# Performance work log

Measured on AMD Instinct MI355X. Metric: run time of the kernel, lower is better.

## Reference

```python
import jax, jax.numpy as jnp
import numpy as np

T, P, S, A = 16384, 64, 128, 16
VD, VO, TD, TO, H = 1024, 256, 768, 256, 512

def _mlp1(x, w1, b1, w2, b2):
    # MLP1: Linear(d,d) -> ReLU -> Linear(d,out)
    return jax.nn.relu(x @ w1 + b1) @ w2 + b2

def setup_inputs() -> dict:
    key = jax.random.key(0)
    ks = jax.random.split(key, 20)
    p = lambda i, shape: jax.random.normal(ks[i], shape, jnp.float32) * 0.02
    return {
        "video": jax.random.normal(ks[0], (T, VD), jnp.float32),
        "para": jax.random.normal(ks[1], (P, TD), jnp.float32),
        "question": jax.random.normal(ks[2], (1, TD), jnp.float32),
        "paras_score": jax.random.normal(ks[3], (P,), jnp.float32),
        "a_texts": jax.random.normal(ks[4], (S, A, TD), jnp.float32),
        "a_buttons": jax.random.normal(ks[5], (S, A, VD), jnp.float32),
        "timestamps": jnp.sort(jax.random.randint(ks[6], (P, 2), 0, T), axis=1),
        # mlp_v: VD -> VD -> VO
        "wv1": p(7, (VD, VD)), "bv1": jnp.zeros(VD, jnp.float32),
        "wv2": p(8, (VD, VO)), "bv2": jnp.zeros(VO, jnp.float32),
        # mlp_t: TD -> TD -> TO
        "wt1": p(9, (TD, TD)), "bt1": jnp.zeros(TD, jnp.float32),
        "wt2": p(10, (TD, TO)), "bt2": jnp.zeros(TO, jnp.float32),
        # mlp_pre: (2*VO+2*TO) -> same -> H
        "wp1": p(11, (2*VO+2*TO, 2*VO+2*TO)), "bp1": jnp.zeros(2*VO+2*TO, jnp.float32),
        "wp2": p(12, (2*VO+2*TO, H)), "bp2": jnp.zeros(H, jnp.float32),
        # GRUCell H -> H (torch layout: [3H, H])
        "w_ih": p(13, (3*H, H)), "b_ih": jnp.zeros(3*H, jnp.float32),
        "w_hh": p(14, (3*H, H)), "b_hh": jnp.zeros(3*H, jnp.float32),
        # proj: H -> H -> 1
        "wj1": p(15, (H, H)), "bj1": jnp.zeros(H, jnp.float32),
        "wj2": p(16, (H, 1)), "bj2": jnp.zeros(1, jnp.float32),
        "state0": jax.random.normal(ks[17], (H,), jnp.float32),
    }

def reference(video, para, question, paras_score, a_texts, a_buttons, timestamps,
              wv1, bv1, wv2, bv2, wt1, bt1, wt2, bt2, wp1, bp1, wp2, bp2,
              w_ih, b_ih, w_hh, b_hh, wj1, bj1, wj2, bj2, state0):
    score = jax.nn.softmax(paras_score)                       # [P]
    video_v = _mlp1(video, wv1, bv1, wv2, bv2)                # [T, VO]
    # segment mean pooling over ragged [start, end) spans; start>=end -> single frame
    s = timestamps[:, 0]
    e = jnp.maximum(timestamps[:, 1], s + 1)
    idx = jnp.arange(video.shape[0])
    mask = ((idx[None, :] >= s[:, None]) & (idx[None, :] < e[:, None])).astype(video_v.dtype)  # [P, T]
    seg = (mask @ video_v) / (e - s).astype(video_v.dtype)[:, None]  # [P, VO]
    video_seg = score @ seg                                   # [VO]
    text_seg = score @ _mlp1(para, wt1, bt1, wt2, bt2)        # [TO]
    q = _mlp1(question, wt1, bt1, wt2, bt2)                   # [1, TO]
    qa = q[None] + _mlp1(a_texts, wt1, bt1, wt2, bt2)         # [S, A, TO]
    btn = _mlp1(a_buttons, wv1, bv1, wv2, bv2)                # [S, A, VO]
    Sn, An = qa.shape[0], qa.shape[1]
    vb = jnp.broadcast_to(video_seg, (Sn, An, video_seg.shape[0]))
    tb = jnp.broadcast_to(text_seg, (Sn, An, text_seg.shape[0]))
    inputs_pre = _mlp1(jnp.concatenate([vb, tb, qa, btn], axis=-1), wp1, bp1, wp2, bp2)  # [S, A, H]

    def step(state, x):  # x: [A, H]
        h = jnp.broadcast_to(state, x.shape)
        gi = x @ w_ih.T + b_ih
        gh = h @ w_hh.T + b_hh
        ir, iz, inn = jnp.split(gi, 3, axis=-1)
        hr, hz, hn = jnp.split(gh, 3, axis=-1)
        r = jax.nn.sigmoid(ir + hr)
        z = jax.nn.sigmoid(iz + hz)
        n = jnp.tanh(inn + r * hn)
        h_new = (1.0 - z) * n + z * h                          # [A, H]
        logits = _mlp1(h_new, wj1, bj1, wj2, bj2)[:, 0]        # [A]
        new_state = x[jnp.argmax(logits)]                      # history 'max' update
        return new_state, logits

    _, scores = jax.lax.scan(step, state0, inputs_pre)
    return scores  # [S, A]
```

## Files before the change

kernel.cpp:

```cpp
#include <hip/hip_runtime.h>
#include <math.h>

#define T_FRAMES 16384
#define S_N   128
#define VD    1024
#define VO    256
#define TD    768
#define TO    256
#define HH    512
#define NTXT  2113
#define NCAND 32528
#define NGRP  2033
#define NASC  2049
#define MVB   18432

typedef __attribute__((ext_vector_type(8))) short s8v;
typedef __attribute__((ext_vector_type(4))) short s4v;
typedef __attribute__((ext_vector_type(4))) float f32x4;

__device__ __forceinline__ float bf2f(short h) {
    return __builtin_bit_cast(float, ((unsigned)(unsigned short)h) << 16);
}
__device__ __forceinline__ void split_rn(float v, short& h, short& l) {
    unsigned u = __builtin_bit_cast(unsigned, v);
    unsigned short uh = (unsigned short)((u + 0x7fff + ((u >> 16) & 1)) >> 16);
    float lf = v - bf2f((short)uh);
    unsigned ul = __builtin_bit_cast(unsigned, lf);
    unsigned short us = (unsigned short)((ul + 0x7fff + ((ul >> 16) & 1)) >> 16);
    h = (short)uh; l = (short)us;
}
__device__ __forceinline__ void gload16(const void* g, void* l) {
    __builtin_amdgcn_global_load_lds(
        (const __attribute__((address_space(1))) unsigned int*)g,
        (__attribute__((address_space(3))) unsigned int*)l, 16, 0, 0);
}
__device__ __forceinline__ f32x4 ld4s(const short* __restrict__ H,
                                      const short* __restrict__ L, size_t o) {
    s4v h = *(const s4v*)(H + o);
    s4v l = *(const s4v*)(L + o);
    return (f32x4){bf2f(h[0]) + bf2f(l[0]), bf2f(h[1]) + bf2f(l[1]),
                   bf2f(h[2]) + bf2f(l[2]), bf2f(h[3]) + bf2f(l[3])};
}
__device__ __forceinline__ float sigm(float x) { return 1.f / (1.f + expf(-x)); }

struct GD {
    const short *Ah, *Al, *Bh, *Bl;
    const float *bias;
    short *Ch, *Cl;
    int M, N, K, gx, nblk, relu;
};

template<int MODE, int BKL>
__global__ __launch_bounds__((BKL == 64 ? 512 : 256), 2) void mgemm3(
    GD d0, GD d1,
    const float* __restrict__ wt, float* __restrict__ uacc,
    const float* __restrict__ wj2, float* __restrict__ LG)
{
    constexpr int NTH = (BKL == 64) ? 512 : 256;
    constexpr int GPR = BKL / 8;
    constexpr int TSH = 128 * BKL;
    constexpr int MF  = (BKL == 64) ? 2 : 4;
    constexpr int WMs = MF * 16;
    __shared__ __align__(16) short lds[2 * 4 * TSH];

    const int tid = threadIdx.x;
    const int nwg = gridDim.x;
    const int orig = blockIdx.x;
    const int qq = nwg >> 3, r8 = nwg & 7, xcd = orig & 7, ridx = orig >> 3;
    const int swz = (xcd < r8 ? xcd * (qq + 1) : r8 * (qq + 1) + (xcd - r8) * qq) + ridx;

    GD d; int pid;
    if (swz < d0.nblk) { d = d0; pid = swz; } else { d = d1; pid = swz - d0.nblk; }
    const int bm = (pid / d.gx) * 128;
    const int bn = (pid % d.gx) * 128;

    const int wv = tid >> 6, l = tid & 63;
    const int fr = l & 15, fg = l >> 4;
    const int wr = wv >> 1, wc = wv & 1;

    f32x4 acc[MF][4];
#pragma unroll
    for (int m = 0; m < MF; ++m)
#pragma unroll
        for (int n = 0; n < 4; ++n) acc[m][n] = (f32x4){0.f, 0.f, 0.f, 0.f};

    auto stage = [&](int buf, int k0) {
        short* base = &lds[buf * 4 * TSH];
#pragma unroll
        for (int i = 0; i < (128 * GPR) / NTH; ++i) {
            int g = i * NTH + tid;
            int row = g / GPR, c = g % GPR;
            int cs = (BKL == 32) ? (c ^ ((row >> 1) & 3)) : (c ^ (row & 7));
            int ga = bm + row; if (ga > d.M - 1) ga = d.M - 1;
            size_t ao = (size_t)ga * d.K + k0 + cs * 8;
            size_t bo = (size_t)(bn + row) * d.K + k0 + cs * 8;
            gload16(d.Ah + ao, base + 0 * TSH + g * 8);
            gload16(d.Al + ao, base + 1 * TSH + g * 8);
            gload16(d.Bh + bo, base + 2 * TSH + g * 8);
            gload16(d.Bl + bo, base + 3 * TSH + g * 8);
        }
    };
    auto compute = [&](int buf) {
        const short* base = &lds[buf * 4 * TSH];
#pragma unroll
        for (int s = 0; s < BKL / 32; ++s) {
            s8v ah[MF], al[MF];
#pragma unroll
            for (int m = 0; m < MF; ++m) {
                int row = wr * WMs + m * 16 + fr;
                int sw = (BKL == 32) ? ((row >> 1) & 3) : (row & 7);
                int off = row * BKL + (((s << 2) + fg) ^ sw) * 8;
                ah[m] = *(const s8v*)&base[0 * TSH + off];
                al[m] = *(const s8v*)&base[1 * TSH + off];
            }
#pragma unroll
            for (int n = 0; n < 4; ++n) {
                int col = wc * 64 + n * 16 + fr;
                int sw = (BKL == 32) ? ((col >> 1) & 3) : (col & 7);
                int off = col * BKL + (((s << 2) + fg) ^ sw) * 8;
                s8v bh = *(const s8v*)&base[2 * TSH + off];
                s8v bl = *(const s8v*)&base[3 * TSH + off];
#pragma unroll
                for (int m = 0; m < MF; ++m) {
                    f32x4 c = acc[m][n];
                    c = __builtin_amdgcn_mfma_f32_16x16x32_bf16(al[m], bh, c, 0, 0, 0);
                    c = __builtin_amdgcn_mfma_f32_16x16x32_bf16(ah[m], bl, c, 0, 0, 0);
                    c = __builtin_amdgcn_mfma_f32_16x16x32_bf16(ah[m], bh, c, 0, 0, 0);
                    acc[m][n] = c;
                }
            }
        }
    };

    stage(0, 0);
    __syncthreads();
    const int nk = d.K / BKL;
    int cur = 0;
    for (int t = 0; t < nk; ++t) {
        if (t + 1 < nk) stage(cur ^ 1, (t + 1) * BKL);
        compute(cur);
        __syncthreads();
        cur ^= 1;
    }

    if (MODE == 2 && bm < 16384) {
        float wtv[MF][4];
#pragma unroll
        for (int m = 0; m < MF; ++m)
#pragma unroll
            for (int r = 0; r < 4; ++r)
                wtv[m][r] = wt[bm + wr * WMs + m * 16 + fg * 4 + r];
#pragma unroll
        for (int n = 0; n < 4; ++n) {
            int gcol = bn + wc * 64 + n * 16 + fr;
            float bv = d.bias[gcol];
            float s = 0.f;
#pragma unroll
            for (int m = 0; m < MF; ++m)
#pragma unroll
                for (int r = 0; r < 4; ++r)
                    s += fmaxf(acc[m][n][r] + bv, 0.f) * wtv[m][r];
            s += __shfl_xor(s, 16);
            s += __shfl_xor(s, 32);
            if (fg == 0) atomicAdd(&uacc[gcol], s);
        }
        return;
    }
    if (MODE == 3) {
#pragma unroll
        for (int m = 0; m < MF; ++m) {
            float sv[4] = {0.f, 0.f, 0.f, 0.f};
#pragma unroll
            for (int n = 0; n < 4; ++n) {
                int gcol = bn + wc * 64 + n * 16 + fr;
                float bv = d.bias[gcol], w2 = wj2[gcol];
#pragma unroll
                for (int r = 0; r < 4; ++r)
                    sv[r] += fmaxf(acc[m][n][r] + bv, 0.f) * w2;
            }
#pragma unroll
            for (int r = 0; r < 4; ++r) {
                float v = sv[r];
                v += __shfl_xor(v, 1); v += __shfl_xor(v, 2);
                v += __shfl_xor(v, 4); v += __shfl_xor(v, 8);
                int gm = bm + wr * WMs + m * 16 + fg * 4 + r;
                if (fr == 0 && gm < d.M) atomicAdd(&LG[gm], v);
            }
        }
        return;
    }
    {
        const int rowoff = (MODE == 2) ? 16384 : 0;
#pragma unroll
        for (int n = 0; n < 4; ++n) {
            int gcol = bn + wc * 64 + n * 16 + fr;
            float bv = d.bias[gcol];
#pragma unroll
            for (int m = 0; m < MF; ++m) {
                int rbase = bm + wr * WMs + m * 16 + fg * 4;
#pragma unroll
                for (int r = 0; r < 4; ++r) {
                    int gm = rbase + r;
                    if (gm < d.M) {
                        float v = acc[m][n][r] + bv;
                        if (d.relu || MODE == 2) v = fmaxf(v, 0.f);
                        short hh, ll; split_rn(v, hh, ll);
                        size_t o = (size_t)(gm - rowoff) * d.N + gcol;
                        d.Ch[o] = hh; d.Cl[o] = ll;
                    }
                }
            }
        }
    }
}

struct PrepArgs {
    const float* src[9];
    short* dh[9]; short* dl[9];
    int K[9], N[9], tr[9];
};
__global__ __launch_bounds__(256) void prep_weights(PrepArgs a)
{
    const int wi = blockIdx.y;
    const float* src = a.src[wi];
    short* dh = a.dh[wi]; short* dl = a.dl[wi];
    const int K = a.K[wi], N = a.N[wi];
    __shared__ float t[32][33];
    if (a.tr[wi]) {
        int nb = N >> 5, kb = K >> 5;
        if ((int)blockIdx.x >= nb * kb) return;
        int tx = threadIdx.x & 31, ty = threadIdx.x >> 5;
        int n0 = ((int)blockIdx.x % nb) << 5, k0 = ((int)blockIdx.x / nb) << 5;
#pragma unroll
        for (int i = 0; i < 4; ++i)
            t[ty + 8 * i][tx] = src[(size_t)(k0 + ty + 8 * i) * N + n0 + tx];
        __syncthreads();
#pragma unroll
        for (int i = 0; i < 4; ++i) {
            int n = n0 + ty + 8 * i, k = k0 + tx;
            short h, l; split_rn(t[tx][ty + 8 * i], h, l);
            dh[(size_t)n * K + k] = h;
            dl[(size_t)n * K + k] = l;
        }
    } else {
        int total = K * N;
        int i0 = ((int)blockIdx.x * 256 + (int)threadIdx.x) * 4;
        if (i0 < total) {
            float4 v = *(const float4*)(src + i0);
            float vv[4] = {v.x, v.y, v.z, v.w};
#pragma unroll
            for (int e = 0; e < 4; ++e) {
                short h, l; split_rn(vv[e], h, l);
                dh[i0 + e] = h; dl[i0 + e] = l;
            }
        }
    }
}

__global__ __launch_bounds__(256) void asplit_vb(const float* __restrict__ video,
                                                 const float* __restrict__ btns,
                                                 short* __restrict__ h,
                                                 short* __restrict__ l)
{
    const size_t vtotal = (size_t)16384 * VD;
    const size_t total = (size_t)MVB * VD;
    for (size_t i = ((size_t)blockIdx.x * 256 + threadIdx.x) * 4; i < total;
         i += (size_t)gridDim.x * 1024) {
        const float* s = (i < vtotal) ? video + i : btns + (i - vtotal);
        float4 v = *(const float4*)s;
        float vv[4] = {v.x, v.y, v.z, v.w};
#pragma unroll
        for (int e = 0; e < 4; ++e) {
            short hh, ll; split_rn(vv[e], hh, ll);
            h[i + e] = hh; l[i + e] = ll;
        }
    }
}

__global__ __launch_bounds__(256) void prolog(const float* __restrict__ ps,
                                              float* __restrict__ sc,
                                              float* __restrict__ u,
                                              const float* __restrict__ state0,
                                              short* __restrict__ ASCh,
                                              short* __restrict__ ASCl,
                                              const float* __restrict__ bj2,
                                              float* __restrict__ LG)
{
    int b = blockIdx.x, tid = threadIdx.x;
    if (b == 0) {
        if (tid < 64) {
            float x = ps[tid];
            float m = x;
            for (int off = 32; off; off >>= 1) m = fmaxf(m, __shfl_xor(m, off));
            float e = expf(x - m);
            float s = e;
            for (int off = 32; off; off >>= 1) s += __shfl_xor(s, off);
            sc[tid] = e / s;
        }
    } else if (b == 1) {
#pragma unroll
        for (int i = 0; i < 4; ++i) u[tid + i * 256] = 0.f;
    } else if (b == 2) {
#pragma unroll
        for (int i = 0; i < 2; ++i) {
            int c = tid + i * 256;
            short h, l; split_rn(state0[c], h, l);
            ASCh[c] = h; ASCl[c] = l;
        }
    } else {
        int i = (b - 3) * 256 + tid;
        if (i < NCAND) LG[i] = bj2[0];
    }
}

__global__ __launch_bounds__(256) void wt_kernel(const int* __restrict__ ts,
                                                 const float* __restrict__ sc,
                                                 float* __restrict__ wt)
{
    __shared__ int ss[64], se[64];
    __shared__ float sw[64];
    int tid = threadIdx.x;
    if (tid < 64) {
        int s = ts[2 * tid];
        int e = ts[2 * tid + 1];
        if (e < s + 1) e = s + 1;
        ss[tid] = s; se[tid] = e;
        sw[tid] = sc[tid] / (float)(e - s);
    }
    __syncthreads();
    int t = blockIdx.x * 256 + tid;
    if (t < T_FRAMES) {
        float w = 0.f;
#pragma unroll
        for (int p = 0; p < 64; ++p)
            if (t >= ss[p] && t < se[p]) w += sw[p];
        wt[t] = w;
    }
}

__global__ __launch_bounds__(256) void mkbias2(const float* __restrict__ u,
                                               const float* __restrict__ wv2,
                                               const float* __restrict__ bv2,
                                               const float* __restrict__ sc,
                                               const short* __restrict__ T2h,
                                               const short* __restrict__ T2l,
                                               const float* __restrict__ bp1,
                                               const float* __restrict__ wp1,
                                               float* __restrict__ bias2)
{
    __shared__ float vs[256], ts[256];
    int tid = threadIdx.x;
    float a = 0.f;
    for (int p = 0; p < 64; ++p) {
        size_t o = (size_t)p * TO + tid;
        a = fmaf(sc[p], bf2f(T2h[o]) + bf2f(T2l[o]), a);
    }
    ts[tid] = a;
    float b = bv2[tid];
    for (int i = 0; i < VD; ++i)
        b = fmaf(u[i], wv2[(size_t)i * VO + tid], b);
    vs[tid] = b;
    __syncthreads();
    int j = blockIdx.x * 256 + tid;
    float acc = bp1[j];
    for (int i = 0; i < 256; ++i) acc = fmaf(vs[i], wp1[(size_t)i * 1024 + j], acc);
    for (int i = 0; i < 256; ++i) acc = fmaf(ts[i], wp1[(size_t)(256 + i) * 1024 + j], acc);
    bias2[j] = acc;
}

__global__ __launch_bounds__(256) void copy_xt_split(const float* __restrict__ para,
                                                     const float* __restrict__ question,
                                                     const float* __restrict__ atexts,
                                                     short* __restrict__ Xh,
                                                     short* __restrict__ Xl)
{
    size_t total = (size_t)NTXT * TD;
    for (size_t id = ((size_t)blockIdx.x * 256 + threadIdx.x) * 4; id < total;
         id += (size_t)gridDim.x * 1024) {
        int r = (int)(id / TD);
        int c = (int)(id - (size_t)r * TD);
        const float* s;
        if (r < 64)       s = para + (size_t)r * TD + c;
        else if (r == 64) s = question + c;
        else              s = atexts + (size_t)(r - 65) * TD + c;
        float4 v = *(const float4*)s;
        float vv[4] = {v.x, v.y, v.z, v.w};
#pragma unroll
        for (int e = 0; e < 4; ++e) {
            short h, l; split_rn(vv[e], h, l);
            Xh[id + e] = h; Xl[id + e] = l;
        }
    }
}

__global__ __launch_bounds__(256) void xp_build_split(const short* __restrict__ T2h,
                                                      const short* __restrict__ T2l,
                                                      const short* __restrict__ btnh,
                                                      const short* __restrict__ btnl,
                                                      short* __restrict__ Xh,
                                                      short* __restrict__ Xl)
{
    int idx = blockIdx.x * 256 + threadIdx.x;
    int r = idx >> 7;
    int c = (idx & 127) << 2;
    s4v h, l;
    if (c < 256) {
        size_t o1 = (size_t)64 * TO + c;
        size_t o2 = (size_t)(65 + r) * TO + c;
        s4v h1 = *(const s4v*)(T2h + o1), l1 = *(const s4v*)(T2l + o1);
        s4v h2 = *(const s4v*)(T2h + o2), l2 = *(const s4v*)(T2l + o2);
#pragma unroll
        for (int e = 0; e < 4; ++e) {
            float v = (bf2f(h1[e]) + bf2f(l1[e])) + (bf2f(h2[e]) + bf2f(l2[e]));
            short hh, ll; split_rn(v, hh, ll);
            h[e] = hh; l[e] = ll;
        }
    } else {
        size_t o = (size_t)r * VO + (c - 256);
        h = *(const s4v*)(btnh + o);
        l = *(const s4v*)(btnl + o);
    }
    size_t out = (size_t)r * 512 + c;
    *(s4v*)(Xh + out) = h;
    *(s4v*)(Xl + out) = l;
}

__global__ __launch_bounds__(256) void hn_build(const short* __restrict__ GIh,
                                                const short* __restrict__ GIl,
                                                const short* __restrict__ GHh,
                                                const short* __restrict__ GHl,
                                                const short* __restrict__ ASCh,
                                                const short* __restrict__ ASCl,
                                                short* __restrict__ HNh,
                                                short* __restrict__ HNl)
{
    const int total = NCAND * 128;
    for (int gid = blockIdx.x * 256 + threadIdx.x; gid < total;
         gid += gridDim.x * 256) {
        int r = gid >> 7;
        int c = (gid & 127) << 2;
        int crow, girow;
        if (r < 16) { crow = 0; girow = r; }
        else {
            int rr = r - 16;
            int k  = 1 + (rr >> 8);
            int rem = rr & 255;
            int ci = rem >> 4;
            int aa = rem & 15;
            crow = 1 + (k - 1) * 16 + ci;
            girow = k * 16 + aa;
        }
        size_t gi0 = (size_t)girow * 1536 + c;
        size_t gh0 = (size_t)crow * 1536 + c;
        f32x4 ir = ld4s(GIh, GIl, gi0);
        f32x4 iz = ld4s(GIh, GIl, gi0 + 512);
        f32x4 in = ld4s(GIh, GIl, gi0 + 1024);
        f32x4 hr = ld4s(GHh, GHl, gh0);
        f32x4 hz = ld4s(GHh, GHl, gh0 + 512);
        f32x4 hn = ld4s(GHh, GHl, gh0 + 1024);
        f32x4 h  = ld4s(ASCh, ASCl, (size_t)crow * HH + c);
        s4v oh, ol;
#pragma unroll
        for (int e = 0; e < 4; ++e) {
            float rg = sigm(ir[e] + hr[e]);
            float z  = sigm(iz[e] + hz[e]);
            float n  = tanhf(in[e] + rg * hn[e]);
            float v  = (1.f - z) * n + z * h[e];
            short hh, ll; split_rn(v, hh, ll);
            oh[e] = hh; ol[e] = ll;
        }
        size_t out = (size_t)r * HH + c;
        *(s4v*)(HNh + out) = oh;
        *(s4v*)(HNl + out) = ol;
    }
}

__global__ __launch_bounds__(256) void argmax16(const float* __restrict__ LG,
                                                int* __restrict__ idx)
{
    int g = blockIdx.x * 4 + (threadIdx.x >> 6);
    if (g >= NGRP) return;
    int lane = threadIdx.x & 63;
    float v = (lane < 16) ? LG[g * 16 + lane] : -INFINITY;
    int bi = (lane < 16) ? lane : 16;
    for (int off = 8; off >= 1; off >>= 1) {
        float ov = __shfl_xor(v, off);
        int   oi = __shfl_xor(bi, off);
        if (ov > v || (ov == v && oi < bi)) { v = ov; bi = oi; }
    }
    if (lane == 0) idx[g] = bi;
}

__global__ void chase2(const float* __restrict__ LG, const int* __restrict__ idx,
                       float* __restrict__ out)
{
    int lane = threadIdx.x;
    int g = 0;
    for (int k = 0; k < S_N; ++k) {
        if (lane < 16) out[k * 16 + lane] = LG[g * 16 + lane];
        int ci = idx[g];
        g = 1 + k * 16 + ci;
    }
}

extern "C" void kernel_launch(void* const* d_in, const int* in_sizes, int n_in,
                              void* d_out, int out_size, void* d_ws, size_t ws_size,
                              hipStream_t stream)
{
    const float* video      = (const float*)d_in[0];
    const float* para       = (const float*)d_in[1];
    const float* question   = (const float*)d_in[2];
    const float* paras_scr  = (const float*)d_in[3];
    const float* a_texts    = (const float*)d_in[4];
    const float* a_buttons  = (const float*)d_in[5];
    const int*   timestamps = (const int*)d_in[6];
    const float* wv1 = (const float*)d_in[7];
    const float* bv1 = (const float*)d_in[8];
    const float* wv2 = (const float*)d_in[9];
    const float* bv2 = (const float*)d_in[10];
    const float* wt1 = (const float*)d_in[11];
    const float* bt1 = (const float*)d_in[12];
    const float* wt2 = (const float*)d_in[13];
    const float* bt2 = (const float*)d_in[14];
    const float* wp1 = (const float*)d_in[15];
    const float* bp1 = (const float*)d_in[16];
    const float* wp2 = (const float*)d_in[17];
    const float* bp2 = (const float*)d_in[18];
    const float* w_ih = (const float*)d_in[19];
    const float* b_ih = (const float*)d_in[20];
    const float* w_hh = (const float*)d_in[21];
    const float* b_hh = (const float*)d_in[22];
    const float* wj1 = (const float*)d_in[23];
    const float* bj1 = (const float*)d_in[24];
    const float* wj2 = (const float*)d_in[25];
    const float* bj2 = (const float*)d_in[26];
    const float* state0 = (const float*)d_in[27];

    char* wsb = (char*)d_ws;
    size_t off = 0;
    auto alloc = [&](size_t bytes) -> char* {
        size_t o = (off + 255) & ~(size_t)255;
        off = o + bytes;
        return wsb + o;
    };
    auto allocF = [&](size_t n) -> float* { return (float*)alloc(n * 4); };
    auto allocS = [&](size_t n) -> short* { return (short*)alloc(n * 2); };
    auto allocI = [&](size_t n) -> int*   { return (int*)alloc(n * 4); };

    float* sc    = allocF(64);
    float* wtb   = allocF(T_FRAMES);
    float* u     = allocF(VD);
    float* bias2 = allocF(1024);
    float* LG    = allocF(NCAND);
    int*   amx   = allocI(NGRP);

    short* Avbh = allocS((size_t)MVB * VD);
    short* Avbl = allocS((size_t)MVB * VD);
    short* H1bh = allocS((size_t)2048 * VD);
    short* H1bl = allocS((size_t)2048 * VD);
    short* Xth  = allocS((size_t)NTXT * TD);
    short* Xtl  = allocS((size_t)NTXT * TD);
    short* T1h  = allocS((size_t)NTXT * TD);
    short* T1l  = allocS((size_t)NTXT * TD);
    short* T2h  = allocS((size_t)NTXT * TO);
    short* T2l  = allocS((size_t)NTXT * TO);
    short* btnh = allocS((size_t)2048 * VO);
    short* btnl = allocS((size_t)2048 * VO);
    short* Xph  = allocS((size_t)2048 * 512);
    short* Xpl  = allocS((size_t)2048 * 512);
    short* P1h  = allocS((size_t)2048 * 1024);
    short* P1l  = allocS((size_t)2048 * 1024);
    short* ASCh = allocS((size_t)NASC * HH);
    short* ASCl = allocS((size_t)NASC * HH);
    short* GIh  = allocS((size_t)2048 * 1536);
    short* GIl  = allocS((size_t)2048 * 1536);
    short* GHh  = allocS((size_t)NASC * 1536);
    short* GHl  = allocS((size_t)NASC * 1536);
    short* IPh  = ASCh + HH;
    short* IPl  = ASCl + HH;
    short* HNh  = Avbh;
    short* HNl  = Avbl;

    short* wv1Th = allocS((size_t)VD * VD);    short* wv1Tl = allocS((size_t)VD * VD);
    short* wt1Th = allocS((size_t)TD * TD);    short* wt1Tl = allocS((size_t)TD * TD);
    short* wt2Th = allocS((size_t)TO * TD);    short* wt2Tl = allocS((size_t)TO * TD);
    short* wv2Th = allocS((size_t)VO * VD);    short* wv2Tl = allocS((size_t)VO * VD);
    short* wp1Th = allocS((size_t)1024 * 512); short* wp1Tl = allocS((size_t)1024 * 512);
    short* wp2Th = allocS((size_t)HH * 1024);  short* wp2Tl = allocS((size_t)HH * 1024);
    short* wj1Th = allocS((size_t)HH * HH);    short* wj1Tl = allocS((size_t)HH * HH);
    short* wihSh = allocS((size_t)1536 * HH);  short* wihSl = allocS((size_t)1536 * HH);
    short* whhSh = allocS((size_t)1536 * HH);  short* whhSl = allocS((size_t)1536 * HH);

    GD gE; gE.Ah = gE.Al = gE.Bh = gE.Bl = nullptr; gE.bias = nullptr;
    gE.Ch = gE.Cl = nullptr; gE.M = gE.N = gE.K = gE.gx = gE.nblk = gE.relu = 0;

    prolog<<<131, 256, 0, stream>>>(paras_scr, sc, u, state0, ASCh, ASCl, bj2, LG);
    wt_kernel<<<T_FRAMES / 256, 256, 0, stream>>>(timestamps, sc, wtb);
    {
        PrepArgs pa;
        const float* s[9] = {wv1, wt1, wt2, wv2, wp1 + (size_t)512 * 1024, wp2, wj1, w_ih, w_hh};
        short* dh[9] = {wv1Th, wt1Th, wt2Th, wv2Th, wp1Th, wp2Th, wj1Th, wihSh, whhSh};
        short* dl[9] = {wv1Tl, wt1Tl, wt2Tl, wv2Tl, wp1Tl, wp2Tl, wj1Tl, wihSl, whhSl};
        int K[9] = {VD, TD, TD, VD, 512, 1024, HH, HH, HH};
        int N[9] = {VD, TD, TO, VO, 1024, HH, HH, 1536, 1536};
        int tr[9] = {1, 1, 1, 1, 1, 1, 1, 0, 0};
        for (int i = 0; i < 9; ++i) {
            pa.src[i] = s[i]; pa.dh[i] = dh[i]; pa.dl[i] = dl[i];
            pa.K[i] = K[i]; pa.N[i] = N[i]; pa.tr[i] = tr[i];
        }
        prep_weights<<<dim3(1024, 9), 256, 0, stream>>>(pa);
    }
    asplit_vb<<<4608, 256, 0, stream>>>(video, a_buttons, Avbh, Avbl);
    copy_xt_split<<<1586, 256, 0, stream>>>(para, question, a_texts, Xth, Xtl);

    {
        GD g1{Avbh, Avbl, wv1Th, wv1Tl, bv1, H1bh, H1bl, MVB, VD, VD, 8, 1152, 1};
        mgemm3<2, 32><<<1152, 256, 0, stream>>>(g1, gE, wtb, u, nullptr, nullptr);
    }
    {
        GD g2{H1bh, H1bl, wv2Th, wv2Tl, bv2, btnh, btnl, 2048, VO, VD, 2, 32, 0};
        GD g3{Xth, Xtl, wt1Th, wt1Tl, bt1, T1h, T1l, NTXT, TD, TD, 6, 102, 1};
        mgemm3<0, 64><<<134, 512, 0, stream>>>(g2, g3, nullptr, nullptr, nullptr, nullptr);
    }
    {
        GD g4{T1h, T1l, wt2Th, wt2Tl, bt2, T2h, T2l, NTXT, TO, TD, 2, 34, 0};
        mgemm3<0, 64><<<34, 512, 0, stream>>>(g4, gE, nullptr, nullptr, nullptr, nullptr);
    }
    mkbias2<<<4, 256, 0, stream>>>(u, wv2, bv2, sc, T2h, T2l, bp1, wp1, bias2);
    xp_build_split<<<1024, 256, 0, stream>>>(T2h, T2l, btnh, btnl, Xph, Xpl);
    {
        GD g5{Xph, Xpl, wp1Th, wp1Tl, bias2, P1h, P1l, 2048, 1024, 512, 8, 128, 1};
        mgemm3<0, 64><<<128, 512, 0, stream>>>(g5, gE, nullptr, nullptr, nullptr, nullptr);
    }
    {
        GD g6{P1h, P1l, wp2Th, wp2Tl, bp2, IPh, IPl, 2048, HH, 1024, 4, 64, 0};
        mgemm3<0, 64><<<64, 512, 0, stream>>>(g6, gE, nullptr, nullptr, nullptr, nullptr);
    }
    {
        GD g7{IPh, IPl, wihSh, wihSl, b_ih, GIh, GIl, 2048, 1536, HH, 12, 192, 0};
        GD g8{ASCh, ASCl, whhSh, whhSl, b_hh, GHh, GHl, NASC, 1536, HH, 12, 204, 0};
        mgemm3<0, 64><<<396, 512, 0, stream>>>(g7, g8, nullptr, nullptr, nullptr, nullptr);
    }
    hn_build<<<4096, 256, 0, stream>>>(GIh, GIl, GHh, GHl, ASCh, ASCl, HNh, HNl);
    {
        GD g9{HNh, HNl, wj1Th, wj1Tl, bj1, nullptr, nullptr, NCAND, HH, HH, 4, 1020, 0};
        mgemm3<3, 32><<<1020, 256, 0, stream>>>(g9, gE, nullptr, nullptr, wj2, LG);
    }
    argmax16<<<(NGRP + 3) / 4, 256, 0, stream>>>(LG, amx);
    chase2<<<1, 64, 0, stream>>>(LG, amx, (float*)d_out);
}
```

Baseline: 656.9 us.

## Merge independent GEMM launches, parallelize bias precompute, single-buffer BK32 GEMM

Turns the GEMM epilogue mode into a runtime field so GEMMs with different epilogues share one launch: the big video MLP layer now runs alongside the text first layer, and the wv2/wt2 GEMMs share another launch. The serial mkbias2 kernel becomes two wave-parallel kernels (mkseg, bias2k) that read the pre-split transposed bf16 weights, and the full wp1 is transposed with a leading-dimension offset. The BK=32 path drops double buffering for single-buffered LDS to improve occupancy, the wj1 GEMM moves to the BK=64 variant, and chase2 caches argmax indices in shared memory. These remove launch serialization and slow scalar loops, at the cost of runtime branching in the epilogue and a loss of load/compute overlap in the BK=32 path.

```diff
diff --git a/kernel.cpp b/kernel.cpp
--- a/kernel.cpp
+++ b/kernel.cpp
@@ -47,21 +47,22 @@
     const short *Ah, *Al, *Bh, *Bl;
     const float *bias;
     short *Ch, *Cl;
-    int M, N, K, gx, nblk, relu;
+    int M, N, K, lda, ldb, gx, nblk, mode;
 };
 
-template<int MODE, int BKL>
-__global__ __launch_bounds__((BKL == 64 ? 512 : 256), 2) void mgemm3(
+template<int BKL>
+__global__ __launch_bounds__((BKL == 64 ? 512 : 256), 2) void gemmk(
     GD d0, GD d1,
     const float* __restrict__ wt, float* __restrict__ uacc,
     const float* __restrict__ wj2, float* __restrict__ LG)
 {
-    constexpr int NTH = (BKL == 64) ? 512 : 256;
-    constexpr int GPR = BKL / 8;
-    constexpr int TSH = 128 * BKL;
-    constexpr int MF  = (BKL == 64) ? 2 : 4;
-    constexpr int WMs = MF * 16;
-    __shared__ __align__(16) short lds[2 * 4 * TSH];
+    constexpr int NTH  = (BKL == 64) ? 512 : 256;
+    constexpr int GPR  = BKL / 8;
+    constexpr int TSH  = 128 * BKL;
+    constexpr int MF   = (BKL == 64) ? 2 : 4;
+    constexpr int WMs  = MF * 16;
+    constexpr int NBUF = (BKL == 64) ? 2 : 1;
+    __shared__ __align__(16) short lds[NBUF * 4 * TSH];
 
     const int tid = threadIdx.x;
     const int nwg = gridDim.x;
@@ -92,8 +93,8 @@
             int row = g / GPR, c = g % GPR;
             int cs = (BKL == 32) ? (c ^ ((row >> 1) & 3)) : (c ^ (row & 7));
             int ga = bm + row; if (ga > d.M - 1) ga = d.M - 1;
-            size_t ao = (size_t)ga * d.K + k0 + cs * 8;
-            size_t bo = (size_t)(bn + row) * d.K + k0 + cs * 8;
+            size_t ao = (size_t)ga * d.lda + k0 + cs * 8;
+            size_t bo = (size_t)(bn + row) * d.ldb + k0 + cs * 8;
             gload16(d.Ah + ao, base + 0 * TSH + g * 8);
             gload16(d.Al + ao, base + 1 * TSH + g * 8);
             gload16(d.Bh + bo, base + 2 * TSH + g * 8);
@@ -132,18 +133,27 @@
         }
     };
 
-    stage(0, 0);
-    __syncthreads();
     const int nk = d.K / BKL;
-    int cur = 0;
-    for (int t = 0; t < nk; ++t) {
-        if (t + 1 < nk) stage(cur ^ 1, (t + 1) * BKL);
-        compute(cur);
+    if (NBUF == 1) {
+        for (int t = 0; t < nk; ++t) {
+            stage(0, t * BKL);
+            __syncthreads();
+            compute(0);
+            __syncthreads();
+        }
+    } else {
+        stage(0, 0);
         __syncthreads();
-        cur ^= 1;
-    }
-
-    if (MODE == 2 && bm < 16384) {
+        int cur = 0;
+        for (int t = 0; t < nk; ++t) {
+            if (t + 1 < nk) stage(cur ^ 1, (t + 1) * BKL);
+            compute(cur);
+            __syncthreads();
+            cur ^= 1;
+        }
+    }
+
+    if (d.mode == 2 && bm < 16384) {
         float wtv[MF][4];
 #pragma unroll
         for (int m = 0; m < MF; ++m)
@@ -166,7 +176,7 @@
         }
         return;
     }
-    if (MODE == 3) {
+    if (d.mode == 3) {
 #pragma unroll
         for (int m = 0; m < MF; ++m) {
             float sv[4] = {0.f, 0.f, 0.f, 0.f};
@@ -190,7 +200,8 @@
         return;
     }
     {
-        const int rowoff = (MODE == 2) ? 16384 : 0;
+        const int rowoff = (d.mode == 2) ? 16384 : 0;
+        const bool dorelu = (d.mode >= 1);
 #pragma unroll
         for (int n = 0; n < 4; ++n) {
             int gcol = bn + wc * 64 + n * 16 + fr;
@@ -203,7 +214,7 @@
                     int gm = rbase + r;
                     if (gm < d.M) {
                         float v = acc[m][n][r] + bv;
-                        if (d.relu || MODE == 2) v = fmaxf(v, 0.f);
+                        if (dorelu) v = fmaxf(v, 0.f);
                         short hh, ll; split_rn(v, hh, ll);
                         size_t o = (size_t)(gm - rowoff) * d.N + gcol;
                         d.Ch[o] = hh; d.Cl[o] = ll;
@@ -338,34 +349,64 @@
     }
 }
 
-__global__ __launch_bounds__(256) void mkbias2(const float* __restrict__ u,
-                                               const float* __restrict__ wv2,
-                                               const float* __restrict__ bv2,
-                                               const float* __restrict__ sc,
-                                               const short* __restrict__ T2h,
-                                               const short* __restrict__ T2l,
-                                               const float* __restrict__ bp1,
-                                               const float* __restrict__ wp1,
-                                               float* __restrict__ bias2)
-{
-    __shared__ float vs[256], ts[256];
-    int tid = threadIdx.x;
-    float a = 0.f;
-    for (int p = 0; p < 64; ++p) {
-        size_t o = (size_t)p * TO + tid;
-        a = fmaf(sc[p], bf2f(T2h[o]) + bf2f(T2l[o]), a);
-    }
-    ts[tid] = a;
-    float b = bv2[tid];
-    for (int i = 0; i < VD; ++i)
-        b = fmaf(u[i], wv2[(size_t)i * VO + tid], b);
-    vs[tid] = b;
-    __syncthreads();
-    int j = blockIdx.x * 256 + tid;
-    float acc = bp1[j];
-    for (int i = 0; i < 256; ++i) acc = fmaf(vs[i], wp1[(size_t)i * 1024 + j], acc);
-    for (int i = 0; i < 256; ++i) acc = fmaf(ts[i], wp1[(size_t)(256 + i) * 1024 + j], acc);
-    bias2[j] = acc;
+__global__ __launch_bounds__(256) void mkseg(const float* __restrict__ u,
+                                             const short* __restrict__ wh,
+                                             const short* __restrict__ wl,
+                                             const float* __restrict__ bv2,
+                                             const float* __restrict__ sc,
+                                             const short* __restrict__ T2h,
+                                             const short* __restrict__ T2l,
+                                             float* __restrict__ segc)
+{
+    int b = blockIdx.x;
+    if (b < 64) {
+        int j = b * 4 + (threadIdx.x >> 6);
+        int lane = threadIdx.x & 63;
+        const s8v* ph = (const s8v*)(wh + (size_t)j * VD + lane * 16);
+        const s8v* pl = (const s8v*)(wl + (size_t)j * VD + lane * 16);
+        const float4* pu = (const float4*)(u + lane * 16);
+        float acc = 0.f;
+#pragma unroll
+        for (int qq = 0; qq < 2; ++qq) {
+            s8v h = ph[qq], l = pl[qq];
+            float4 u0 = pu[qq * 2], u1 = pu[qq * 2 + 1];
+            float uu[8] = {u0.x, u0.y, u0.z, u0.w, u1.x, u1.y, u1.z, u1.w};
+#pragma unroll
+            for (int e = 0; e < 8; ++e)
+                acc = fmaf(uu[e], bf2f(h[e]) + bf2f(l[e]), acc);
+        }
+        for (int off = 32; off; off >>= 1) acc += __shfl_xor(acc, off);
+        if (lane == 0) segc[j] = acc + bv2[j];
+    } else {
+        int j = threadIdx.x;
+        float acc = 0.f;
+        for (int p = 0; p < 64; ++p) {
+            size_t o = (size_t)p * TO + j;
+            acc = fmaf(sc[p], bf2f(T2h[o]) + bf2f(T2l[o]), acc);
+        }
+        segc[256 + j] = acc;
+    }
+}
+
+__global__ __launch_bounds__(256) void bias2k(const float* __restrict__ segc,
+                                              const short* __restrict__ wp1Th,
+                                              const short* __restrict__ wp1Tl,
+                                              const float* __restrict__ bp1,
+                                              float* __restrict__ bias2)
+{
+    int j = blockIdx.x * 4 + (threadIdx.x >> 6);
+    int lane = threadIdx.x & 63;
+    s8v h = *(const s8v*)(wp1Th + (size_t)j * 1024 + lane * 8);
+    s8v l = *(const s8v*)(wp1Tl + (size_t)j * 1024 + lane * 8);
+    const float4* ps = (const float4*)(segc + lane * 8);
+    float4 s0 = ps[0], s1 = ps[1];
+    float sv[8] = {s0.x, s0.y, s0.z, s0.w, s1.x, s1.y, s1.z, s1.w};
+    float acc = 0.f;
+#pragma unroll
+    for (int e = 0; e < 8; ++e)
+        acc = fmaf(sv[e], bf2f(h[e]) + bf2f(l[e]), acc);
+    for (int off = 32; off; off >>= 1) acc += __shfl_xor(acc, off);
+    if (lane == 0) bias2[j] = acc + bp1[j];
 }
 
 __global__ __launch_bounds__(256) void copy_xt_split(const float* __restrict__ para,
@@ -494,11 +535,14 @@
 __global__ void chase2(const float* __restrict__ LG, const int* __restrict__ idx,
                        float* __restrict__ out)
 {
+    __shared__ int sidx[NGRP];
     int lane = threadIdx.x;
+    for (int i = lane; i < NGRP; i += 64) sidx[i] = idx[i];
+    __syncthreads();
     int g = 0;
     for (int k = 0; k < S_N; ++k) {
         if (lane < 16) out[k * 16 + lane] = LG[g * 16 + lane];
-        int ci = idx[g];
+        int ci = sidx[g];
         g = 1 + k * 16 + ci;
     }
 }
@@ -550,6 +594,7 @@
     float* sc    = allocF(64);
     float* wtb   = allocF(T_FRAMES);
     float* u     = allocF(VD);
+    float* segc  = allocF(512);
     float* bias2 = allocF(1024);
     float* LG    = allocF(NCAND);
     int*   amx   = allocI(NGRP);
@@ -581,27 +626,28 @@
     short* HNh  = Avbh;
     short* HNl  = Avbl;
 
-    short* wv1Th = allocS((size_t)VD * VD);    short* wv1Tl = allocS((size_t)VD * VD);
-    short* wt1Th = allocS((size_t)TD * TD);    short* wt1Tl = allocS((size_t)TD * TD);
-    short* wt2Th = allocS((size_t)TO * TD);    short* wt2Tl = allocS((size_t)TO * TD);
-    short* wv2Th = allocS((size_t)VO * VD);    short* wv2Tl = allocS((size_t)VO * VD);
-    short* wp1Th = allocS((size_t)1024 * 512); short* wp1Tl = allocS((size_t)1024 * 512);
-    short* wp2Th = allocS((size_t)HH * 1024);  short* wp2Tl = allocS((size_t)HH * 1024);
-    short* wj1Th = allocS((size_t)HH * HH);    short* wj1Tl = allocS((size_t)HH * HH);
-    short* wihSh = allocS((size_t)1536 * HH);  short* wihSl = allocS((size_t)1536 * HH);
-    short* whhSh = allocS((size_t)1536 * HH);  short* whhSl = allocS((size_t)1536 * HH);
+    short* wv1Th = allocS((size_t)VD * VD);     short* wv1Tl = allocS((size_t)VD * VD);
+    short* wt1Th = allocS((size_t)TD * TD);     short* wt1Tl = allocS((size_t)TD * TD);
+    short* wt2Th = allocS((size_t)TO * TD);     short* wt2Tl = allocS((size_t)TO * TD);
+    short* wv2Th = allocS((size_t)VO * VD);     short* wv2Tl = allocS((size_t)VO * VD);
+    short* wp1Th = allocS((size_t)1024 * 1024); short* wp1Tl = allocS((size_t)1024 * 1024);
+    short* wp2Th = allocS((size_t)HH * 1024);   short* wp2Tl = allocS((size_t)HH * 1024);
+    short* wj1Th = allocS((size_t)HH * HH);     short* wj1Tl = allocS((size_t)HH * HH);
+    short* wihSh = allocS((size_t)1536 * HH);   short* wihSl = allocS((size_t)1536 * HH);
+    short* whhSh = allocS((size_t)1536 * HH);   short* whhSl = allocS((size_t)1536 * HH);
 
     GD gE; gE.Ah = gE.Al = gE.Bh = gE.Bl = nullptr; gE.bias = nullptr;
-    gE.Ch = gE.Cl = nullptr; gE.M = gE.N = gE.K = gE.gx = gE.nblk = gE.relu = 0;
+    gE.Ch = gE.Cl = nullptr; gE.M = gE.N = gE.K = gE.lda = gE.ldb = 0;
+    gE.gx = 1; gE.nblk = 0; gE.mode = 0;
 
     prolog<<<131, 256, 0, stream>>>(paras_scr, sc, u, state0, ASCh, ASCl, bj2, LG);
     wt_kernel<<<T_FRAMES / 256, 256, 0, stream>>>(timestamps, sc, wtb);
     {
         PrepArgs pa;
-        const float* s[9] = {wv1, wt1, wt2, wv2, wp1 + (size_t)512 * 1024, wp2, wj1, w_ih, w_hh};
+        const float* s[9] = {wv1, wt1, wt2, wv2, wp1, wp2, wj1, w_ih, w_hh};
         short* dh[9] = {wv1Th, wt1Th, wt2Th, wv2Th, wp1Th, wp2Th, wj1Th, wihSh, whhSh};
         short* dl[9] = {wv1Tl, wt1Tl, wt2Tl, wv2Tl, wp1Tl, wp2Tl, wj1Tl, wihSl, whhSl};
-        int K[9] = {VD, TD, TD, VD, 512, 1024, HH, HH, HH};
+        int K[9] = {VD, TD, TD, VD, 1024, 1024, HH, HH, HH};
         int N[9] = {VD, TD, TO, VO, 1024, HH, HH, 1536, 1536};
         int tr[9] = {1, 1, 1, 1, 1, 1, 1, 0, 0};
         for (int i = 0; i < 9; ++i) {
@@ -614,37 +660,36 @@
     copy_xt_split<<<1586, 256, 0, stream>>>(para, question, a_texts, Xth, Xtl);
 
     {
-        GD g1{Avbh, Avbl, wv1Th, wv1Tl, bv1, H1bh, H1bl, MVB, VD, VD, 8, 1152, 1};
-        mgemm3<2, 32><<<1152, 256, 0, stream>>>(g1, gE, wtb, u, nullptr, nullptr);
-    }
-    {
-        GD g2{H1bh, H1bl, wv2Th, wv2Tl, bv2, btnh, btnl, 2048, VO, VD, 2, 32, 0};
-        GD g3{Xth, Xtl, wt1Th, wt1Tl, bt1, T1h, T1l, NTXT, TD, TD, 6, 102, 1};
-        mgemm3<0, 64><<<134, 512, 0, stream>>>(g2, g3, nullptr, nullptr, nullptr, nullptr);
-    }
-    {
-        GD g4{T1h, T1l, wt2Th, wt2Tl, bt2, T2h, T2l, NTXT, TO, TD, 2, 34, 0};
-        mgemm3<0, 64><<<34, 512, 0, stream>>>(g4, gE, nullptr, nullptr, nullptr, nullptr);
-    }
-    mkbias2<<<4, 256, 0, stream>>>(u, wv2, bv2, sc, T2h, T2l, bp1, wp1, bias2);
+        GD g1{Avbh, Avbl, wv1Th, wv1Tl, bv1, H1bh, H1bl, MVB, VD, VD, VD, VD, 8, 1152, 2};
+        GD g3{Xth, Xtl, wt1Th, wt1Tl, bt1, T1h, T1l, NTXT, TD, TD, TD, TD, 6, 102, 1};
+        gemmk<32><<<1254, 256, 0, stream>>>(g1, g3, wtb, u, nullptr, nullptr);
+    }
+    {
+        GD g2{H1bh, H1bl, wv2Th, wv2Tl, bv2, btnh, btnl, 2048, VO, VD, VD, VD, 2, 32, 0};
+        GD g4{T1h, T1l, wt2Th, wt2Tl, bt2, T2h, T2l, NTXT, TO, TD, TD, TD, 2, 34, 0};
+        gemmk<64><<<66, 512, 0, stream>>>(g2, g4, nullptr, nullptr, nullptr, nullptr);
+    }
+    mkseg<<<65, 256, 0, stream>>>(u, wv2Th, wv2Tl, bv2, sc, T2h, T2l, segc);
+    bias2k<<<256, 256, 0, stream>>>(segc, wp1Th, wp1Tl, bp1, bias2);
     xp_build_split<<<1024, 256, 0, stream>>>(T2h, T2l, btnh, btnl, Xph, Xpl);
     {
-        GD g5{Xph, Xpl, wp1Th, wp1Tl, bias2, P1h, P1l, 2048, 1024, 512, 8, 128, 1};
-        mgemm3<0, 64><<<128, 512, 0, stream>>>(g5, gE, nullptr, nullptr, nullptr, nullptr);
-    }
-    {
-        GD g6{P1h, P1l, wp2Th, wp2Tl, bp2, IPh, IPl, 2048, HH, 1024, 4, 64, 0};
-        mgemm3<0, 64><<<64, 512, 0, stream>>>(g6, gE, nullptr, nullptr, nullptr, nullptr);
-    }
-    {
-        GD g7{IPh, IPl, wihSh, wihSl, b_ih, GIh, GIl, 2048, 1536, HH, 12, 192, 0};
-        GD g8{ASCh, ASCl, whhSh, whhSl, b_hh, GHh, GHl, NASC, 1536, HH, 12, 204, 0};
-        mgemm3<0, 64><<<396, 512, 0, stream>>>(g7, g8, nullptr, nullptr, nullptr, nullptr);
+        GD g5{Xph, Xpl, wp1Th + 512, wp1Tl + 512, bias2, P1h, P1l,
+              2048, 1024, 512, 512, 1024, 8, 128, 1};
+        gemmk<64><<<128, 512, 0, stream>>>(g5, gE, nullptr, nullptr, nullptr, nullptr);
+    }
+    {
+        GD g6{P1h, P1l, wp2Th, wp2Tl, bp2, IPh, IPl, 2048, HH, 1024, 1024, 1024, 4, 64, 0};
+        gemmk<64><<<64, 512, 0, stream>>>(g6, gE, nullptr, nullptr, nullptr, nullptr);
+    }
+    {
+        GD g7{IPh, IPl, wihSh, wihSl, b_ih, GIh, GIl, 2048, 1536, HH, HH, HH, 12, 192, 0};
+        GD g8{ASCh, ASCl, whhSh, whhSl, b_hh, GHh, GHl, NASC, 1536, HH, HH, HH, 12, 204, 0};
+        gemmk<64><<<396, 512, 0, stream>>>(g7, g8, nullptr, nullptr, nullptr, nullptr);
     }
     hn_build<<<4096, 256, 0, stream>>>(GIh, GIl, GHh, GHl, ASCh, ASCl, HNh, HNl);
     {
-        GD g9{HNh, HNl, wj1Th, wj1Tl, bj1, nullptr, nullptr, NCAND, HH, HH, 4, 1020, 0};
-        mgemm3<3, 32><<<1020, 256, 0, stream>>>(g9, gE, nullptr, nullptr, wj2, LG);
+        GD g9{HNh, HNl, wj1Th, wj1Tl, bj1, nullptr, nullptr, NCAND, HH, HH, HH, HH, 4, 1020, 3};
+        gemmk<64><<<1020, 512, 0, stream>>>(g9, gE, nullptr, nullptr, wj2, LG);
     }
     argmax16<<<(NGRP + 3) / 4, 256, 0, stream>>>(LG, amx);
     chase2<<<1, 64, 0, stream>>>(LG, amx, (float*)d_out);
```

Result: faster. 571.0 us (-13.1%).
